# Optimization experiments

Hardware: AMD Instinct MI355X
Metric: run time of the kernel (lower is better)

The kernel has to match this reference:

```python
import jax, jax.numpy as jnp
import numpy as np

NUM_CLASSES = 21
THRESHOLD = 0.5
VAR0, VAR1 = 0.1, 0.2
NEGPOS_RATIO = 3


def setup_inputs() -> dict:
    key = jax.random.key(0)
    k1, k2, k3, k4, k5, k6, k7 = jax.random.split(key, 7)
    B, P, C, O = 64, 8732, 21, 8
    loc_data = jax.random.normal(k1, (B, P, 4), dtype=jnp.float32) * 0.1
    conf_data = jax.random.normal(k2, (B, P, C), dtype=jnp.float32)
    # priors: center form (cx, cy, w, h), valid in [0,1]
    cxy = jax.random.uniform(k3, (P, 2), minval=0.05, maxval=0.95)
    pwh = jax.random.uniform(k4, (P, 2), minval=0.05, maxval=0.3)
    priors = jnp.concatenate([cxy, pwh], axis=-1).astype(jnp.float32)
    # targets: corner-form boxes + class label (float), (B, O, 5)
    tc = jax.random.uniform(k5, (B, O, 2), minval=0.2, maxval=0.8)
    twh = jax.random.uniform(k6, (B, O, 2), minval=0.1, maxval=0.4)
    tmin = jnp.clip(tc - twh / 2, 0.0, 1.0)
    tmax = jnp.clip(tc + twh / 2, 0.0, 1.0)
    labels = jax.random.randint(k7, (B, O, 1), 0, C - 1).astype(jnp.float32)
    targets = jnp.concatenate([tmin, tmax, labels], axis=-1)
    return {"loc_data": loc_data, "conf_data": conf_data, "priors": priors, "targets": targets}


def _point_form(p):
    # (cx,cy,w,h) -> (xmin,ymin,xmax,ymax)
    return jnp.concatenate([p[:, :2] - p[:, 2:] / 2, p[:, :2] + p[:, 2:] / 2], axis=-1)


def _jaccard(a, b):
    # a: (O,4) corners, b: (P,4) corners -> (O,P)
    lt = jnp.maximum(a[:, None, :2], b[None, :, :2])
    rb = jnp.minimum(a[:, None, 2:], b[None, :, 2:])
    wh = jnp.clip(rb - lt, 0.0, None)
    inter = wh[..., 0] * wh[..., 1]
    area_a = ((a[:, 2] - a[:, 0]) * (a[:, 3] - a[:, 1]))[:, None]
    area_b = ((b[:, 2] - b[:, 0]) * (b[:, 3] - b[:, 1]))[None, :]
    return inter / (area_a + area_b - inter)


def _match_one(truths, labels, priors_pt, priors):
    # truths: (O,4) corners, labels: (O,), priors: (P,4) center-form
    ov = _jaccard(truths, priors_pt)                      # (O,P)
    best_prior_idx = jnp.argmax(ov, axis=1)               # (O,)
    best_truth_overlap = jnp.max(ov, axis=0)              # (P,)
    best_truth_idx = jnp.argmax(ov, axis=0)               # (P,)
    # ensure every gt box matches its best prior
    best_truth_overlap = best_truth_overlap.at[best_prior_idx].set(2.0)
    best_truth_idx = best_truth_idx.at[best_prior_idx].set(jnp.arange(truths.shape[0]))
    matched = truths[best_truth_idx]                      # (P,4)
    conf = labels[best_truth_idx].astype(jnp.int32) + 1
    conf = jnp.where(best_truth_overlap < THRESHOLD, 0, conf)
    # encode offsets
    g_cxcy = ((matched[:, :2] + matched[:, 2:]) / 2 - priors[:, :2]) / (VAR0 * priors[:, 2:])
    g_wh = jnp.log(jnp.clip((matched[:, 2:] - matched[:, :2]) / priors[:, 2:], 1e-8, None)) / VAR1
    return jnp.concatenate([g_cxcy, g_wh], axis=-1), conf


def _forward(loc_data, conf_data, priors, targets):
    B, P, C = conf_data.shape
    priors_sg = jax.lax.stop_gradient(priors)             # torch uses .data
    targets_sg = jax.lax.stop_gradient(targets)
    priors_pt = _point_form(priors_sg)
    loc_t, conf_t = jax.vmap(_match_one, in_axes=(0, 0, None, None))(
        targets_sg[:, :, :4], targets_sg[:, :, 4], priors_pt, priors_sg)
    pos = conf_t > 0                                      # (B,P)

    # localization: smooth L1 summed over positive priors
    diff = loc_data - loc_t
    ad = jnp.abs(diff)
    sl1 = jnp.where(ad < 1.0, 0.5 * diff * diff, ad - 0.5)
    loss_l = jnp.sum(sl1 * pos[..., None].astype(sl1.dtype))

    # per-prior conf loss for hard negative mining
    lse = jax.nn.logsumexp(conf_data, axis=-1)            # (B,P)
    gathered = jnp.take_along_axis(conf_data, conf_t[..., None], axis=-1)[..., 0]
    loss_c_all = lse - gathered                           # (B,P)
    mined = jnp.where(pos, 0.0, loss_c_all)
    loss_idx = jnp.argsort(-mined, axis=1)                # descending
    idx_rank = jnp.argsort(loss_idx, axis=1)
    num_pos = jnp.sum(pos.astype(jnp.int32), axis=1, keepdims=True)  # (B,1)
    num_neg = jnp.minimum(NEGPOS_RATIO * num_pos, P - num_pos)
    neg = idx_rank < num_neg                              # (B,P)

    sel = (pos | neg).astype(loss_c_all.dtype)
    loss_c = jnp.sum(loss_c_all * sel)

    N = jnp.sum(num_pos).astype(loss_l.dtype)
    return loss_l / N, loss_c / N


def reference(loc_data, conf_data, priors, targets):
    return _forward(loc_data, conf_data, priors, targets)
```

## Files before the change

kernel.cpp:

```cpp
#include <hip/hip_runtime.h>
#include <math.h>

#define TPB 256
#define CHP 512
#define TPBS 1024
#define RCAP 12

typedef unsigned long long ull;
typedef float pf4 __attribute__((ext_vector_type(4), aligned(4)));

__device__ __forceinline__ float jac(float tx0, float ty0, float tx1, float ty1, float ta,
                                     float px0, float py0, float px1, float py1, float pa) {
    float ltx = fmaxf(tx0, px0), lty = fmaxf(ty0, py0);
    float rbx = fminf(tx1, px1), rby = fminf(ty1, py1);
    float w = fmaxf(rbx - ltx, 0.0f), h = fmaxf(rby - lty, 0.0f);
    float inter = w * h;
    return inter / (ta + pa - inter);
}

template <int ON>
__global__ __launch_bounds__(TPB) void match1_kernel(
    const float* __restrict__ priors, const float* __restrict__ targets,
    int P, int O_rt, int S1, ull* __restrict__ pkeys) {
    constexpr int OMAX = (ON > 0) ? ON : 64;
    const int O = (ON > 0) ? ON : O_rt;
    const int b = blockIdx.x / S1;
    const int chunk = blockIdx.x % S1;
    const int p0 = chunk * CHP;
    const int p1 = min(p0 + CHP, P);
    const int tid = threadIdx.x;
    const int lane = tid & 63, wv = tid >> 6;

    __shared__ float s_tx0[OMAX], s_ty0[OMAX], s_tx1[OMAX], s_ty1[OMAX], s_area[OMAX];
    __shared__ ull s_wk[TPB / 64][OMAX];
    for (int o = tid; o < O; o += TPB) {
        const float* t = targets + ((size_t)b * O + o) * 5;
        float x0 = t[0], y0 = t[1], x1 = t[2], y1 = t[3];
        s_tx0[o] = x0; s_ty0[o] = y0; s_tx1[o] = x1; s_ty1[o] = y1;
        s_area[o] = (x1 - x0) * (y1 - y0);
    }
    __syncthreads();

    ull k[OMAX];
    for (int o = 0; o < O; ++o) k[o] = 0ull;
    for (int p = p0 + tid; p < p1; p += TPB) {
        float4 pr = ((const float4*)priors)[p];
        float px0 = pr.x - pr.z * 0.5f, py0 = pr.y - pr.w * 0.5f;
        float px1 = pr.x + pr.z * 0.5f, py1 = pr.y + pr.w * 0.5f;
        float pa = (px1 - px0) * (py1 - py0);
        for (int o = 0; o < O; ++o) {
            float ov = jac(s_tx0[o], s_ty0[o], s_tx1[o], s_ty1[o], s_area[o],
                           px0, py0, px1, py1, pa);
            ull kk = ((ull)__float_as_uint(ov) << 32) |
                     (ull)(0xFFFFFFFFu - (unsigned)p);
            if (kk > k[o]) k[o] = kk;
        }
    }
    for (int o = 0; o < O; ++o) {
        ull kk = k[o];
        for (int off = 32; off > 0; off >>= 1) {
            ull other = __shfl_down(kk, off, 64);
            if (other > kk) kk = other;
        }
        if (lane == 0) s_wk[wv][o] = kk;
    }
    __syncthreads();
    if (tid < O) {
        ull kk = s_wk[0][tid];
        for (int w = 1; w < TPB / 64; ++w)
            if (s_wk[w][tid] > kk) kk = s_wk[w][tid];
        pkeys[((size_t)b * O + tid) * S1 + chunk] = kk;
    }
}

template <int ON, int CN>
__global__ __launch_bounds__(TPB) void m2c_kernel(
    const float* __restrict__ loc, const float* __restrict__ priors,
    const float* __restrict__ targets, const float* __restrict__ conf,
    const ull* __restrict__ pkeys,
    int P, int O_rt, int C_rt, int S1, int CB2,
    float* __restrict__ mined, float* __restrict__ part_ll,
    float* __restrict__ part_pc, int* __restrict__ part_np) {
    constexpr int OMAX = (ON > 0) ? ON : 64;
    constexpr int CC = (CN > 0) ? CN : 32;
    const int O = (ON > 0) ? ON : O_rt;
    const int C = (CN > 0) ? CN : C_rt;
    const int b = blockIdx.x / CB2;
    const int chunk = blockIdx.x % CB2;
    const int tid = threadIdx.x;
    const int p = chunk * TPB + tid;
    const bool pv = (p < P);

    __shared__ float s_tx0[OMAX], s_ty0[OMAX], s_tx1[OMAX], s_ty1[OMAX];
    __shared__ float s_lab[OMAX], s_area[OMAX];
    __shared__ ull s_keys[OMAX];
    __shared__ int s_bp[OMAX];
    __shared__ float s_wll[TPB / 64], s_wpc[TPB / 64];
    __shared__ int s_wnp[TPB / 64];

    float rv[CC];
    float4 pr4 = make_float4(0.f, 0.f, 1.f, 1.f);
    if (pv) {
        const float* row = conf + ((size_t)b * P + p) * C;
        if (CN > 0) {
#pragma unroll
            for (int q = 0; q < CN / 4; ++q) {
                pf4 v = *(const pf4*)(row + 4 * q);
#pragma unroll
                for (int e = 0; e < 4; ++e) rv[4 * q + e] = v[e];
            }
#pragma unroll
            for (int j = (CN / 4) * 4; j < CN; ++j) rv[j] = row[j];
        } else {
            for (int j = 0; j < C; ++j) rv[j] = row[j];
        }
        pr4 = ((const float4*)priors)[p];
    }

    for (int o = tid; o < O; o += TPB) {
        const float* t = targets + ((size_t)b * O + o) * 5;
        float x0 = t[0], y0 = t[1], x1 = t[2], y1 = t[3];
        s_tx0[o] = x0; s_ty0[o] = y0; s_tx1[o] = x1; s_ty1[o] = y1;
        s_lab[o] = t[4];
        s_area[o] = (x1 - x0) * (y1 - y0);
        s_keys[o] = 0ull;
    }
    __syncthreads();
    if (tid < O * S1) {
        int o = tid / S1, s = tid % S1;
        atomicMax(&s_keys[o], pkeys[((size_t)b * O + o) * S1 + s]);
    }
    __syncthreads();
    if (tid < O)
        s_bp[tid] = (int)(0xFFFFFFFFu - (unsigned)(s_keys[tid] & 0xFFFFFFFFull));
    __syncthreads();

    float ll = 0.0f, pc = 0.0f;
    int np = 0;

    if (pv) {
        float m = rv[0];
#pragma unroll
        for (int j = 1; j < CC; ++j) { if (CN > 0 || j < C) m = fmaxf(m, rv[j]); }
        float s = 0.0f;
#pragma unroll
        for (int j = 0; j < CC; ++j) { if (CN > 0 || j < C) s += expf(rv[j] - m); }
        float lse = m + logf(s);

        float cx = pr4.x, cy = pr4.y, pw = pr4.z, ph = pr4.w;
        float px0 = cx - pw * 0.5f, py0 = cy - ph * 0.5f;
        float px1 = cx + pw * 0.5f, py1 = cy + ph * 0.5f;
        float pa = (px1 - px0) * (py1 - py0);
        float bto = -1.0f;
        int bti = 0;
        for (int o = 0; o < O; ++o) {
            float ov = jac(s_tx0[o], s_ty0[o], s_tx1[o], s_ty1[o], s_area[o],
                           px0, py0, px1, py1, pa);
            if (ov > bto) { bto = ov; bti = o; }
        }
        for (int o = 0; o < O; ++o) {
            if (s_bp[o] == p) { bto = 2.0f; bti = o; }
        }
        int c = (bto < 0.5f) ? 0 : ((int)s_lab[bti] + 1);

        float rowc = rv[0];
#pragma unroll
        for (int j = 1; j < CC; ++j) { if (CN > 0 || j < C) { if (c == j) rowc = rv[j]; } }
        float lc = lse - rowc;

        bool pos = c > 0;
        mined[(size_t)b * P + p] = pos ? 0.0f : lc;
        if (pos) {
            pc = lc;
            np = 1;
            float mx0 = s_tx0[bti], my0 = s_ty0[bti];
            float mx1 = s_tx1[bti], my1 = s_ty1[bti];
            float g0 = ((mx0 + mx1) * 0.5f - cx) / (0.1f * pw);
            float g1 = ((my0 + my1) * 0.5f - cy) / (0.1f * ph);
            float g2 = logf(fmaxf((mx1 - mx0) / pw, 1e-8f)) / 0.2f;
            float g3 = logf(fmaxf((my1 - my0) / ph, 1e-8f)) / 0.2f;
            float4 ld = ((const float4*)loc)[(size_t)b * P + p];
            float gt4[4] = {g0, g1, g2, g3};
            float lv[4] = {ld.x, ld.y, ld.z, ld.w};
#pragma unroll
            for (int q = 0; q < 4; ++q) {
                float d = lv[q] - gt4[q];
                float ad = fabsf(d);
                ll += (ad < 1.0f) ? 0.5f * d * d : (ad - 0.5f);
            }
        }
    }

#pragma unroll
    for (int d = 1; d < 64; d <<= 1) {
        ll += __shfl_xor(ll, d, 64);
        pc += __shfl_xor(pc, d, 64);
        np += __shfl_xor(np, d, 64);
    }
    const int wv = tid >> 6, lane = tid & 63;
    if (lane == 0) { s_wll[wv] = ll; s_wpc[wv] = pc; s_wnp[wv] = np; }
    __syncthreads();
    if (tid == 0) {
        float L = 0.f, Pc = 0.f;
        int N = 0;
        for (int w = 0; w < TPB / 64; ++w) { L += s_wll[w]; Pc += s_wpc[w]; N += s_wnp[w]; }
        part_ll[blockIdx.x] = L;
        part_pc[blockIdx.x] = Pc;
        part_np[blockIdx.x] = N;
    }
}

__global__ __launch_bounds__(TPBS) void select_kernel(
    const float* __restrict__ mined, const float* __restrict__ part_ll,
    const float* __restrict__ part_pc, const int* __restrict__ part_np,
    float* __restrict__ ll_batch, float* __restrict__ lc_batch,
    int* __restrict__ np_batch, int P, int CB, int ratio) {
    const int b = blockIdx.x, tid = threadIdx.x;
    const int lane = tid & 63, wv = tid >> 6;
    constexpr int W = TPBS / 64;
    const float* v = mined + (size_t)b * P;
    const int NIT = (P + TPBS - 1) / TPBS;
    const bool cached = (NIT <= RCAP);

    __shared__ float s_wf[W], s_wg[W];
    __shared__ int s_wi[W];
    __shared__ int s_hist[W * 256];
    __shared__ int s_wt[4];
    __shared__ unsigned s_bsel;
    __shared__ int s_krn;
    __shared__ float s_bc[2];
    __shared__ int s_bn;

    float rv[RCAP];
    if (cached) {
        for (int it = 0; it < NIT; ++it) {
            int p = tid + it * TPBS;
            rv[it] = (p < P) ? v[p] : 0.0f;
        }
    }

    float pll = 0.0f, ppc = 0.0f;
    int pnp = 0;
    for (int i = tid; i < CB; i += TPBS) {
        pll += part_ll[b * CB + i];
        ppc += part_pc[b * CB + i];
        pnp += part_np[b * CB + i];
    }
#pragma unroll
    for (int d = 1; d < 64; d <<= 1) {
        pll += __shfl_xor(pll, d, 64);
        ppc += __shfl_xor(ppc, d, 64);
        pnp += __shfl_xor(pnp, d, 64);
    }
    if (lane == 0) { s_wf[wv] = pll; s_wg[wv] = ppc; s_wi[wv] = pnp; }
    __syncthreads();
    if (tid == 0) {
        float L = 0.f, Pc = 0.f;
        int N = 0;
        for (int w = 0; w < W; ++w) { L += s_wf[w]; Pc += s_wg[w]; N += s_wi[w]; }
        s_bc[0] = L; s_bc[1] = Pc; s_bn = N;
    }
    __syncthreads();
    const float ll_sum = s_bc[0];
    const float sum_pos = s_bc[1];
    const int npos = s_bn;

    const int k = min(ratio * npos, P - npos);
    if (tid == 0) {
        ll_batch[b] = ll_sum;
        np_batch[b] = npos;
    }
    if (k <= 0) {
        if (tid == 0) lc_batch[b] = sum_pos;
        return;
    }

    unsigned prefix = 0u;
    int kr = k;
    for (int pass = 0; pass < 4; ++pass) {
        const int shift = 24 - 8 * pass;
        const unsigned mask = (pass == 0) ? 0u : (0xFFFFFFFFu << (32 - 8 * pass));
        for (int i = tid; i < W * 256; i += TPBS) s_hist[i] = 0;
        __syncthreads();
        for (int it = 0; it < NIT; ++it) {
            int p = tid + it * TPBS;
            if (p < P) {
                unsigned u = __float_as_uint(cached ? rv[it] : v[p]);
                if ((u & mask) == prefix)
                    atomicAdd(&s_hist[wv * 256 + ((u >> shift) & 0xFF)], 1);
            }
        }
        __syncthreads();
        int sge = 0, h = 0;
        if (tid < 256) {
            for (int w = 0; w < W; ++w) h += s_hist[w * 256 + tid];
            int val = h;
#pragma unroll
            for (int d = 1; d < 64; d <<= 1) {
                int t = __shfl_down(val, d, 64);
                if (lane + d < 64) val += t;
            }
            if (lane == 0) s_wt[tid >> 6] = val;
            sge = val;
        }
        __syncthreads();
        if (tid < 256) {
            for (int w = (tid >> 6) + 1; w < 4; ++w) sge += s_wt[w];
            int sgt = sge - h;
            if (sge >= kr && sgt < kr) {
                s_bsel = (unsigned)tid;
                s_krn = kr - sgt;
            }
        }
        __syncthreads();
        prefix |= s_bsel << shift;
        kr = s_krn;
    }
    const float T = __uint_as_float(prefix);
    float lsum = 0.0f;
    int lcnt = 0;
    for (int it = 0; it < NIT; ++it) {
        int p = tid + it * TPBS;
        if (p < P) {
            float x = cached ? rv[it] : v[p];
            if (x > T) { lsum += x; ++lcnt; }
        }
    }
#pragma unroll
    for (int d = 1; d < 64; d <<= 1) {
        lsum += __shfl_xor(lsum, d, 64);
        lcnt += __shfl_xor(lcnt, d, 64);
    }
    if (lane == 0) { s_wf[wv] = lsum; s_wi[wv] = lcnt; }
    __syncthreads();
    if (tid == 0) {
        float S = 0.f;
        int Cn = 0;
        for (int w = 0; w < W; ++w) { S += s_wf[w]; Cn += s_wi[w]; }
        lc_batch[b] = sum_pos + S + (float)(k - Cn) * T;
    }
}

__global__ __launch_bounds__(TPB) void finalize_kernel(
    const float* __restrict__ ll_batch, const int* __restrict__ np_batch,
    const float* __restrict__ lc_batch, int B, float* __restrict__ out) {
    const int tid = threadIdx.x;
    __shared__ float s_l[TPB], s_c[TPB];
    __shared__ int s_n[TPB];
    float l = 0.0f, c = 0.0f;
    int n = 0;
    for (int i = tid; i < B; i += TPB) {
        l += ll_batch[i];
        c += lc_batch[i];
        n += np_batch[i];
    }
    s_l[tid] = l; s_c[tid] = c; s_n[tid] = n;
    __syncthreads();
    for (int s = TPB / 2; s > 0; s >>= 1) {
        if (tid < s) {
            s_l[tid] += s_l[tid + s];
            s_c[tid] += s_c[tid + s];
            s_n[tid] += s_n[tid + s];
        }
        __syncthreads();
    }
    if (tid == 0) {
        float N = (float)s_n[0];
        out[0] = s_l[0] / N;
        out[1] = s_c[0] / N;
    }
}

extern "C" void kernel_launch(void* const* d_in, const int* in_sizes, int n_in,
                              void* d_out, int out_size, void* d_ws, size_t ws_size,
                              hipStream_t stream) {
    const float* loc = (const float*)d_in[0];
    const float* conf = (const float*)d_in[1];
    const float* priors = (const float*)d_in[2];
    const float* targets = (const float*)d_in[3];

    const int P = in_sizes[2] / 4;
    const int B = in_sizes[0] / (P * 4);
    const int C = in_sizes[1] / (in_sizes[0] / 4);
    const int O = in_sizes[3] / (B * 5);
    const size_t BP = (size_t)B * P;
    const int S1 = (P + CHP - 1) / CHP;
    const int CB2 = (P + TPB - 1) / TPB;

    ull* pkeys = (ull*)d_ws;
    float* mined = (float*)(pkeys + (size_t)B * O * S1);
    float* part_ll = mined + BP;
    float* part_pc = part_ll + (size_t)B * CB2;
    int* part_np = (int*)(part_pc + (size_t)B * CB2);
    float* ll_batch = (float*)(part_np + (size_t)B * CB2);
    float* lc_batch = ll_batch + B;
    int* np_batch = (int*)(lc_batch + B);

    if (O == 8) {
        match1_kernel<8><<<B * S1, TPB, 0, stream>>>(priors, targets, P, O, S1, pkeys);
        if (C == 21) {
            m2c_kernel<8, 21><<<B * CB2, TPB, 0, stream>>>(
                loc, priors, targets, conf, pkeys, P, O, C, S1, CB2,
                mined, part_ll, part_pc, part_np);
        } else {
            m2c_kernel<8, 0><<<B * CB2, TPB, 0, stream>>>(
                loc, priors, targets, conf, pkeys, P, O, C, S1, CB2,
                mined, part_ll, part_pc, part_np);
        }
    } else {
        match1_kernel<0><<<B * S1, TPB, 0, stream>>>(priors, targets, P, O, S1, pkeys);
        m2c_kernel<0, 0><<<B * CB2, TPB, 0, stream>>>(
            loc, priors, targets, conf, pkeys, P, O, C, S1, CB2,
            mined, part_ll, part_pc, part_np);
    }

    select_kernel<<<B, TPBS, 0, stream>>>(mined, part_ll, part_pc, part_np,
                                          ll_batch, lc_batch, np_batch, P, CB2, 3);

    finalize_kernel<<<1, TPB, 0, stream>>>(ll_batch, np_batch, lc_batch, B,
                                           (float*)d_out);
}
```

Baseline: 133.1 us.

## Fuse prior matching into conf kernel and patch forced matches in select

The separate match1 pass is removed. The conf/loss kernel now computes the per-truth best-prior keys itself and writes them out per block. The select kernel reduces those keys, applies the forced best-prior assignments as a delta correction to the loss sums, and zeroes those entries in the mined values. The finalize kernel is folded into select through a last-block atomic counter, so two launches and one pass over the priors are dropped. The cost is a more complex correction step: ownership dedup when several truths pick the same prior, an uncached path that rechecks forced priors, and a more intricate grid-wide completion protocol.

Result: slower. 162.1 us (+21.8%).

```diff
diff --git a/kernel.cpp b/kernel.cpp
--- a/kernel.cpp
+++ b/kernel.cpp
@@ -2,7 +2,6 @@
 #include <math.h>
 
 #define TPB 256
-#define CHP 512
 #define TPBS 1024
 #define RCAP 12
 
@@ -18,69 +17,14 @@
     return inter / (ta + pa - inter);
 }
 
-template <int ON>
-__global__ __launch_bounds__(TPB) void match1_kernel(
-    const float* __restrict__ priors, const float* __restrict__ targets,
-    int P, int O_rt, int S1, ull* __restrict__ pkeys) {
-    constexpr int OMAX = (ON > 0) ? ON : 64;
-    const int O = (ON > 0) ? ON : O_rt;
-    const int b = blockIdx.x / S1;
-    const int chunk = blockIdx.x % S1;
-    const int p0 = chunk * CHP;
-    const int p1 = min(p0 + CHP, P);
-    const int tid = threadIdx.x;
-    const int lane = tid & 63, wv = tid >> 6;
-
-    __shared__ float s_tx0[OMAX], s_ty0[OMAX], s_tx1[OMAX], s_ty1[OMAX], s_area[OMAX];
-    __shared__ ull s_wk[TPB / 64][OMAX];
-    for (int o = tid; o < O; o += TPB) {
-        const float* t = targets + ((size_t)b * O + o) * 5;
-        float x0 = t[0], y0 = t[1], x1 = t[2], y1 = t[3];
-        s_tx0[o] = x0; s_ty0[o] = y0; s_tx1[o] = x1; s_ty1[o] = y1;
-        s_area[o] = (x1 - x0) * (y1 - y0);
-    }
-    __syncthreads();
-
-    ull k[OMAX];
-    for (int o = 0; o < O; ++o) k[o] = 0ull;
-    for (int p = p0 + tid; p < p1; p += TPB) {
-        float4 pr = ((const float4*)priors)[p];
-        float px0 = pr.x - pr.z * 0.5f, py0 = pr.y - pr.w * 0.5f;
-        float px1 = pr.x + pr.z * 0.5f, py1 = pr.y + pr.w * 0.5f;
-        float pa = (px1 - px0) * (py1 - py0);
-        for (int o = 0; o < O; ++o) {
-            float ov = jac(s_tx0[o], s_ty0[o], s_tx1[o], s_ty1[o], s_area[o],
-                           px0, py0, px1, py1, pa);
-            ull kk = ((ull)__float_as_uint(ov) << 32) |
-                     (ull)(0xFFFFFFFFu - (unsigned)p);
-            if (kk > k[o]) k[o] = kk;
-        }
-    }
-    for (int o = 0; o < O; ++o) {
-        ull kk = k[o];
-        for (int off = 32; off > 0; off >>= 1) {
-            ull other = __shfl_down(kk, off, 64);
-            if (other > kk) kk = other;
-        }
-        if (lane == 0) s_wk[wv][o] = kk;
-    }
-    __syncthreads();
-    if (tid < O) {
-        ull kk = s_wk[0][tid];
-        for (int w = 1; w < TPB / 64; ++w)
-            if (s_wk[w][tid] > kk) kk = s_wk[w][tid];
-        pkeys[((size_t)b * O + tid) * S1 + chunk] = kk;
-    }
-}
-
 template <int ON, int CN>
-__global__ __launch_bounds__(TPB) void m2c_kernel(
+__global__ __launch_bounds__(TPB) void fused_kernel(
     const float* __restrict__ loc, const float* __restrict__ priors,
     const float* __restrict__ targets, const float* __restrict__ conf,
-    const ull* __restrict__ pkeys,
-    int P, int O_rt, int C_rt, int S1, int CB2,
-    float* __restrict__ mined, float* __restrict__ part_ll,
-    float* __restrict__ part_pc, int* __restrict__ part_np) {
+    int P, int O_rt, int C_rt, int CB2,
+    float* __restrict__ mined, ull* __restrict__ pkeys,
+    float* __restrict__ part_ll, float* __restrict__ part_pc,
+    int* __restrict__ part_np, int* __restrict__ counter) {
     constexpr int OMAX = (ON > 0) ? ON : 64;
     constexpr int CC = (CN > 0) ? CN : 32;
     const int O = (ON > 0) ? ON : O_rt;
@@ -90,11 +34,13 @@
     const int tid = threadIdx.x;
     const int p = chunk * TPB + tid;
     const bool pv = (p < P);
+    const int lane = tid & 63, wv = tid >> 6;
+
+    if (blockIdx.x == 0 && tid == 0) *counter = 0;
 
     __shared__ float s_tx0[OMAX], s_ty0[OMAX], s_tx1[OMAX], s_ty1[OMAX];
     __shared__ float s_lab[OMAX], s_area[OMAX];
-    __shared__ ull s_keys[OMAX];
-    __shared__ int s_bp[OMAX];
+    __shared__ ull s_wk[TPB / 64][OMAX];
     __shared__ float s_wll[TPB / 64], s_wpc[TPB / 64];
     __shared__ int s_wnp[TPB / 64];
 
@@ -123,21 +69,41 @@
         s_tx0[o] = x0; s_ty0[o] = y0; s_tx1[o] = x1; s_ty1[o] = y1;
         s_lab[o] = t[4];
         s_area[o] = (x1 - x0) * (y1 - y0);
-        s_keys[o] = 0ull;
-    }
-    __syncthreads();
-    if (tid < O * S1) {
-        int o = tid / S1, s = tid % S1;
-        atomicMax(&s_keys[o], pkeys[((size_t)b * O + o) * S1 + s]);
-    }
-    __syncthreads();
-    if (tid < O)
-        s_bp[tid] = (int)(0xFFFFFFFFu - (unsigned)(s_keys[tid] & 0xFFFFFFFFull));
-    __syncthreads();
+    }
+    __syncthreads();
+
+    float cx = pr4.x, cy = pr4.y, pw = pr4.z, ph = pr4.w;
+    float px0 = cx - pw * 0.5f, py0 = cy - ph * 0.5f;
+    float px1 = cx + pw * 0.5f, py1 = cy + ph * 0.5f;
+    float pa = (px1 - px0) * (py1 - py0);
+    float bto = -1.0f;
+    int bti = 0;
+    for (int o = 0; o < O; ++o) {
+        ull kk = 0ull;
+        if (pv) {
+            float ov = jac(s_tx0[o], s_ty0[o], s_tx1[o], s_ty1[o], s_area[o],
+                           px0, py0, px1, py1, pa);
+            kk = ((ull)__float_as_uint(ov) << 32) |
+                 (ull)(0xFFFFFFFFu - (unsigned)p);
+            if (ov > bto) { bto = ov; bti = o; }
+        }
+#pragma unroll
+        for (int d = 1; d < 64; d <<= 1) {
+            ull other = __shfl_xor(kk, d, 64);
+            if (other > kk) kk = other;
+        }
+        if (lane == 0) s_wk[wv][o] = kk;
+    }
+    __syncthreads();
+    if (tid < O) {
+        ull kk = s_wk[0][tid];
+        for (int w = 1; w < TPB / 64; ++w)
+            if (s_wk[w][tid] > kk) kk = s_wk[w][tid];
+        pkeys[((size_t)b * O + tid) * CB2 + chunk] = kk;
+    }
 
     float ll = 0.0f, pc = 0.0f;
     int np = 0;
-
     if (pv) {
         float m = rv[0];
 #pragma unroll
@@ -147,22 +113,7 @@
         for (int j = 0; j < CC; ++j) { if (CN > 0 || j < C) s += expf(rv[j] - m); }
         float lse = m + logf(s);
 
-        float cx = pr4.x, cy = pr4.y, pw = pr4.z, ph = pr4.w;
-        float px0 = cx - pw * 0.5f, py0 = cy - ph * 0.5f;
-        float px1 = cx + pw * 0.5f, py1 = cy + ph * 0.5f;
-        float pa = (px1 - px0) * (py1 - py0);
-        float bto = -1.0f;
-        int bti = 0;
-        for (int o = 0; o < O; ++o) {
-            float ov = jac(s_tx0[o], s_ty0[o], s_tx1[o], s_ty1[o], s_area[o],
-                           px0, py0, px1, py1, pa);
-            if (ov > bto) { bto = ov; bti = o; }
-        }
-        for (int o = 0; o < O; ++o) {
-            if (s_bp[o] == p) { bto = 2.0f; bti = o; }
-        }
         int c = (bto < 0.5f) ? 0 : ((int)s_lab[bti] + 1);
-
         float rowc = rv[0];
 #pragma unroll
         for (int j = 1; j < CC; ++j) { if (CN > 0 || j < C) { if (c == j) rowc = rv[j]; } }
@@ -197,7 +148,6 @@
         pc += __shfl_xor(pc, d, 64);
         np += __shfl_xor(np, d, 64);
     }
-    const int wv = tid >> 6, lane = tid & 63;
     if (lane == 0) { s_wll[wv] = ll; s_wpc[wv] = pc; s_wnp[wv] = np; }
     __syncthreads();
     if (tid == 0) {
@@ -210,11 +160,20 @@
     }
 }
 
+template <int ON, int CN>
 __global__ __launch_bounds__(TPBS) void select_kernel(
-    const float* __restrict__ mined, const float* __restrict__ part_ll,
-    const float* __restrict__ part_pc, const int* __restrict__ part_np,
+    const float* __restrict__ mined, const float* __restrict__ conf,
+    const float* __restrict__ loc, const float* __restrict__ priors,
+    const float* __restrict__ targets, const ull* __restrict__ pkeys,
+    const float* __restrict__ part_ll, const float* __restrict__ part_pc,
+    const int* __restrict__ part_np,
     float* __restrict__ ll_batch, float* __restrict__ lc_batch,
-    int* __restrict__ np_batch, int P, int CB, int ratio) {
+    int* __restrict__ np_batch,
+    int P, int O_rt, int C_rt, int CB2, int ratio, int B,
+    int* __restrict__ counter, float* __restrict__ out) {
+    constexpr int OMAX = (ON > 0) ? ON : 64;
+    const int O = (ON > 0) ? ON : O_rt;
+    const int C = (CN > 0) ? CN : C_rt;
     const int b = blockIdx.x, tid = threadIdx.x;
     const int lane = tid & 63, wv = tid >> 6;
     constexpr int W = TPBS / 64;
@@ -222,14 +181,18 @@
     const int NIT = (P + TPBS - 1) / TPBS;
     const bool cached = (NIT <= RCAP);
 
+    __shared__ float s_tx0[OMAX], s_ty0[OMAX], s_tx1[OMAX], s_ty1[OMAX];
+    __shared__ float s_lab[OMAX], s_area[OMAX];
+    __shared__ ull s_keys[OMAX];
+    __shared__ int s_bp[OMAX];
     __shared__ float s_wf[W], s_wg[W];
     __shared__ int s_wi[W];
     __shared__ int s_hist[W * 256];
     __shared__ int s_wt[4];
     __shared__ unsigned s_bsel;
     __shared__ int s_krn;
-    __shared__ float s_bc[2];
-    __shared__ int s_bn;
+    __shared__ float s_bc[2], s_fix[2];
+    __shared__ int s_bn, s_fixn, s_last;
 
     float rv[RCAP];
     if (cached) {
@@ -238,14 +201,42 @@
             rv[it] = (p < P) ? v[p] : 0.0f;
         }
     }
-
     float pll = 0.0f, ppc = 0.0f;
     int pnp = 0;
-    for (int i = tid; i < CB; i += TPBS) {
-        pll += part_ll[b * CB + i];
-        ppc += part_pc[b * CB + i];
-        pnp += part_np[b * CB + i];
-    }
+    for (int i = tid; i < CB2; i += TPBS) {
+        pll += part_ll[b * CB2 + i];
+        ppc += part_pc[b * CB2 + i];
+        pnp += part_np[b * CB2 + i];
+    }
+
+    if (tid < O) {
+        const float* t = targets + ((size_t)b * O + tid) * 5;
+        float x0 = t[0], y0 = t[1], x1 = t[2], y1 = t[3];
+        s_tx0[tid] = x0; s_ty0[tid] = y0; s_tx1[tid] = x1; s_ty1[tid] = y1;
+        s_lab[tid] = t[4];
+        s_area[tid] = (x1 - x0) * (y1 - y0);
+        s_keys[tid] = 0ull;
+    }
+    __syncthreads();
+    if (tid < O * CB2) {
+        int o = tid / CB2, s = tid % CB2;
+        atomicMax(&s_keys[o], pkeys[((size_t)b * O + o) * CB2 + s]);
+    }
+    __syncthreads();
+    if (tid < O)
+        s_bp[tid] = (int)(0xFFFFFFFFu - (unsigned)(s_keys[tid] & 0xFFFFFFFFull));
+    __syncthreads();
+
+    if (cached) {
+        for (int it = 0; it < NIT; ++it) {
+            int p = tid + it * TPBS;
+            if (p < P) {
+                for (int o = 0; o < O; ++o)
+                    if (p == s_bp[o]) rv[it] = 0.0f;
+            }
+        }
+    }
+
 #pragma unroll
     for (int d = 1; d < 64; d <<= 1) {
         pll += __shfl_xor(pll, d, 64);
@@ -253,12 +244,86 @@
         pnp += __shfl_xor(pnp, d, 64);
     }
     if (lane == 0) { s_wf[wv] = pll; s_wg[wv] = ppc; s_wi[wv] = pnp; }
+
+    float dll = 0.0f, dpc = 0.0f;
+    int dnp = 0;
+    if (tid < O) {
+        const int o = tid;
+        const int p = s_bp[o];
+        bool owner = true;
+        for (int o2 = o + 1; o2 < O; ++o2)
+            if (s_bp[o2] == p) owner = false;
+        if (owner) {
+            float4 pr = ((const float4*)priors)[p];
+            float cx = pr.x, cy = pr.y, pw = pr.z, ph = pr.w;
+            float px0 = cx - pw * 0.5f, py0 = cy - ph * 0.5f;
+            float px1 = cx + pw * 0.5f, py1 = cy + ph * 0.5f;
+            float pa = (px1 - px0) * (py1 - py0);
+            float bto = -1.0f;
+            int bti = 0;
+            for (int o2 = 0; o2 < O; ++o2) {
+                float ov = jac(s_tx0[o2], s_ty0[o2], s_tx1[o2], s_ty1[o2], s_area[o2],
+                               px0, py0, px1, py1, pa);
+                if (ov > bto) { bto = ov; bti = o2; }
+            }
+            int c_t = (bto < 0.5f) ? 0 : ((int)s_lab[bti] + 1);
+            const float* row = conf + ((size_t)b * P + p) * C;
+            float m = row[0];
+            for (int j = 1; j < C; ++j) m = fmaxf(m, row[j]);
+            float s = 0.0f;
+            for (int j = 0; j < C; ++j) s += expf(row[j] - m);
+            float lse = m + logf(s);
+            int c_n = (int)s_lab[o] + 1;
+            float lc_n = lse - row[c_n];
+            bool pos_t = c_t > 0;
+            float lc_t = lse - row[c_t];
+            dpc = lc_n - (pos_t ? lc_t : 0.0f);
+            dnp = 1 - (pos_t ? 1 : 0);
+            float4 ld = ((const float4*)loc)[(size_t)b * P + p];
+            float lv[4] = {ld.x, ld.y, ld.z, ld.w};
+            float sl_new = 0.0f, sl_old = 0.0f;
+            {
+                float mx0 = s_tx0[o], my0 = s_ty0[o], mx1 = s_tx1[o], my1 = s_ty1[o];
+                float g[4] = {((mx0 + mx1) * 0.5f - cx) / (0.1f * pw),
+                              ((my0 + my1) * 0.5f - cy) / (0.1f * ph),
+                              logf(fmaxf((mx1 - mx0) / pw, 1e-8f)) / 0.2f,
+                              logf(fmaxf((my1 - my0) / ph, 1e-8f)) / 0.2f};
+                for (int q = 0; q < 4; ++q) {
+                    float d = lv[q] - g[q];
+                    float ad = fabsf(d);
+                    sl_new += (ad < 1.0f) ? 0.5f * d * d : (ad - 0.5f);
+                }
+            }
+            if (pos_t) {
+                float mx0 = s_tx0[bti], my0 = s_ty0[bti], mx1 = s_tx1[bti], my1 = s_ty1[bti];
+                float g[4] = {((mx0 + mx1) * 0.5f - cx) / (0.1f * pw),
+                              ((my0 + my1) * 0.5f - cy) / (0.1f * ph),
+                              logf(fmaxf((mx1 - mx0) / pw, 1e-8f)) / 0.2f,
+                              logf(fmaxf((my1 - my0) / ph, 1e-8f)) / 0.2f};
+                for (int q = 0; q < 4; ++q) {
+                    float d = lv[q] - g[q];
+                    float ad = fabsf(d);
+                    sl_old += (ad < 1.0f) ? 0.5f * d * d : (ad - 0.5f);
+                }
+            }
+            dll = sl_new - sl_old;
+        }
+    }
+    if (wv == 0) {
+#pragma unroll
+        for (int d = 1; d < 64; d <<= 1) {
+            dll += __shfl_xor(dll, d, 64);
+            dpc += __shfl_xor(dpc, d, 64);
+            dnp += __shfl_xor(dnp, d, 64);
+        }
+        if (lane == 0) { s_fix[0] = dll; s_fix[1] = dpc; s_fixn = dnp; }
+    }
     __syncthreads();
     if (tid == 0) {
         float L = 0.f, Pc = 0.f;
         int N = 0;
         for (int w = 0; w < W; ++w) { L += s_wf[w]; Pc += s_wg[w]; N += s_wi[w]; }
-        s_bc[0] = L; s_bc[1] = Pc; s_bn = N;
+        s_bc[0] = L + s_fix[0]; s_bc[1] = Pc + s_fix[1]; s_bn = N + s_fixn;
     }
     __syncthreads();
     const float ll_sum = s_bc[0];
@@ -270,104 +335,120 @@
         ll_batch[b] = ll_sum;
         np_batch[b] = npos;
     }
+
     if (k <= 0) {
         if (tid == 0) lc_batch[b] = sum_pos;
-        return;
-    }
-
-    unsigned prefix = 0u;
-    int kr = k;
-    for (int pass = 0; pass < 4; ++pass) {
-        const int shift = 24 - 8 * pass;
-        const unsigned mask = (pass == 0) ? 0u : (0xFFFFFFFFu << (32 - 8 * pass));
-        for (int i = tid; i < W * 256; i += TPBS) s_hist[i] = 0;
-        __syncthreads();
+    } else {
+        unsigned prefix = 0u;
+        int kr = k;
+        for (int pass = 0; pass < 4; ++pass) {
+            const int shift = 24 - 8 * pass;
+            const unsigned mask = (pass == 0) ? 0u : (0xFFFFFFFFu << (32 - 8 * pass));
+            for (int i = tid; i < W * 256; i += TPBS) s_hist[i] = 0;
+            __syncthreads();
+            for (int it = 0; it < NIT; ++it) {
+                int p = tid + it * TPBS;
+                if (p < P) {
+                    float x;
+                    if (cached) x = rv[it];
+                    else {
+                        x = v[p];
+                        for (int o = 0; o < O; ++o)
+                            if (p == s_bp[o]) x = 0.0f;
+                    }
+                    unsigned u = __float_as_uint(x);
+                    if ((u & mask) == prefix)
+                        atomicAdd(&s_hist[wv * 256 + ((u >> shift) & 0xFF)], 1);
+                }
+            }
+            __syncthreads();
+            int sge = 0, h = 0;
+            if (tid < 256) {
+                for (int w = 0; w < W; ++w) h += s_hist[w * 256 + tid];
+                int val = h;
+#pragma unroll
+                for (int d = 1; d < 64; d <<= 1) {
+                    int t = __shfl_down(val, d, 64);
+                    if (lane + d < 64) val += t;
+                }
+                if (lane == 0) s_wt[tid >> 6] = val;
+                sge = val;
+            }
+            __syncthreads();
+            if (tid < 256) {
+                for (int w = (tid >> 6) + 1; w < 4; ++w) sge += s_wt[w];
+                int sgt = sge - h;
+                if (sge >= kr && sgt < kr) {
+                    s_bsel = (unsigned)tid;
+                    s_krn = kr - sgt;
+                }
+            }
+            __syncthreads();
+            prefix |= s_bsel << shift;
+            kr = s_krn;
+        }
+        const float T = __uint_as_float(prefix);
+        float lsum = 0.0f;
+        int lcnt = 0;
         for (int it = 0; it < NIT; ++it) {
             int p = tid + it * TPBS;
             if (p < P) {
-                unsigned u = __float_as_uint(cached ? rv[it] : v[p]);
-                if ((u & mask) == prefix)
-                    atomicAdd(&s_hist[wv * 256 + ((u >> shift) & 0xFF)], 1);
-            }
-        }
+                float x;
+                if (cached) x = rv[it];
+                else {
+                    x = v[p];
+                    for (int o = 0; o < O; ++o)
+                        if (p == s_bp[o]) x = 0.0f;
+                }
+                if (x > T) { lsum += x; ++lcnt; }
+            }
+        }
+#pragma unroll
+        for (int d = 1; d < 64; d <<= 1) {
+            lsum += __shfl_xor(lsum, d, 64);
+            lcnt += __shfl_xor(lcnt, d, 64);
+        }
+        if (lane == 0) { s_wf[wv] = lsum; s_wi[wv] = lcnt; }
         __syncthreads();
-        int sge = 0, h = 0;
-        if (tid < 256) {
-            for (int w = 0; w < W; ++w) h += s_hist[w * 256 + tid];
-            int val = h;
-#pragma unroll
-            for (int d = 1; d < 64; d <<= 1) {
-                int t = __shfl_down(val, d, 64);
-                if (lane + d < 64) val += t;
-            }
-            if (lane == 0) s_wt[tid >> 6] = val;
-            sge = val;
-        }
+        if (tid == 0) {
+            float S = 0.f;
+            int Cn = 0;
+            for (int w = 0; w < W; ++w) { S += s_wf[w]; Cn += s_wi[w]; }
+            lc_batch[b] = sum_pos + S + (float)(k - Cn) * T;
+        }
+    }
+
+    __threadfence();
+    if (tid == 0) {
+        int old = atomicAdd(counter, 1);
+        s_last = (old == B - 1) ? 1 : 0;
+    }
+    __syncthreads();
+    if (s_last) {
+        __threadfence();
+        float l = 0.0f, c = 0.0f;
+        int n = 0;
+        for (int i = tid; i < B; i += TPBS) {
+            l += ll_batch[i];
+            c += lc_batch[i];
+            n += np_batch[i];
+        }
+#pragma unroll
+        for (int d = 1; d < 64; d <<= 1) {
+            l += __shfl_xor(l, d, 64);
+            c += __shfl_xor(c, d, 64);
+            n += __shfl_xor(n, d, 64);
+        }
+        if (lane == 0) { s_wf[wv] = l; s_wg[wv] = c; s_wi[wv] = n; }
         __syncthreads();
-        if (tid < 256) {
-            for (int w = (tid >> 6) + 1; w < 4; ++w) sge += s_wt[w];
-            int sgt = sge - h;
-            if (sge >= kr && sgt < kr) {
-                s_bsel = (unsigned)tid;
-                s_krn = kr - sgt;
-            }
-        }
-        __syncthreads();
-        prefix |= s_bsel << shift;
-        kr = s_krn;
-    }
-    const float T = __uint_as_float(prefix);
-    float lsum = 0.0f;
-    int lcnt = 0;
-    for (int it = 0; it < NIT; ++it) {
-        int p = tid + it * TPBS;
-        if (p < P) {
-            float x = cached ? rv[it] : v[p];
-            if (x > T) { lsum += x; ++lcnt; }
-        }
-    }
-#pragma unroll
-    for (int d = 1; d < 64; d <<= 1) {
-        lsum += __shfl_xor(lsum, d, 64);
-        lcnt += __shfl_xor(lcnt, d, 64);
-    }
-    if (lane == 0) { s_wf[wv] = lsum; s_wi[wv] = lcnt; }
-    __syncthreads();
-    if (tid == 0) {
-        float S = 0.f;
-        int Cn = 0;
-        for (int w = 0; w < W; ++w) { S += s_wf[w]; Cn += s_wi[w]; }
-        lc_batch[b] = sum_pos + S + (float)(k - Cn) * T;
-    }
-}
-
-__global__ __launch_bounds__(TPB) void finalize_kernel(
-    const float* __restrict__ ll_batch, const int* __restrict__ np_batch,
-    const float* __restrict__ lc_batch, int B, float* __restrict__ out) {
-    const int tid = threadIdx.x;
-    __shared__ float s_l[TPB], s_c[TPB];
-    __shared__ int s_n[TPB];
-    float l = 0.0f, c = 0.0f;
-    int n = 0;
-    for (int i = tid; i < B; i += TPB) {
-        l += ll_batch[i];
-        c += lc_batch[i];
-        n += np_batch[i];
-    }
-    s_l[tid] = l; s_c[tid] = c; s_n[tid] = n;
-    __syncthreads();
-    for (int s = TPB / 2; s > 0; s >>= 1) {
-        if (tid < s) {
-            s_l[tid] += s_l[tid + s];
-            s_c[tid] += s_c[tid + s];
-            s_n[tid] += s_n[tid + s];
-        }
-        __syncthreads();
-    }
-    if (tid == 0) {
-        float N = (float)s_n[0];
-        out[0] = s_l[0] / N;
-        out[1] = s_c[0] / N;
+        if (tid == 0) {
+            float L = 0.f, Cc = 0.f;
+            int N = 0;
+            for (int w = 0; w < W; ++w) { L += s_wf[w]; Cc += s_wg[w]; N += s_wi[w]; }
+            float Nf = (float)N;
+            out[0] = L / Nf;
+            out[1] = Cc / Nf;
+        }
     }
 }
 
@@ -384,39 +465,31 @@
     const int C = in_sizes[1] / (in_sizes[0] / 4);
     const int O = in_sizes[3] / (B * 5);
     const size_t BP = (size_t)B * P;
-    const int S1 = (P + CHP - 1) / CHP;
     const int CB2 = (P + TPB - 1) / TPB;
 
     ull* pkeys = (ull*)d_ws;
-    float* mined = (float*)(pkeys + (size_t)B * O * S1);
+    float* mined = (float*)(pkeys + (size_t)B * O * CB2);
     float* part_ll = mined + BP;
     float* part_pc = part_ll + (size_t)B * CB2;
     int* part_np = (int*)(part_pc + (size_t)B * CB2);
     float* ll_batch = (float*)(part_np + (size_t)B * CB2);
     float* lc_batch = ll_batch + B;
     int* np_batch = (int*)(lc_batch + B);
-
-    if (O == 8) {
-        match1_kernel<8><<<B * S1, TPB, 0, stream>>>(priors, targets, P, O, S1, pkeys);
-        if (C == 21) {
-            m2c_kernel<8, 21><<<B * CB2, TPB, 0, stream>>>(
-                loc, priors, targets, conf, pkeys, P, O, C, S1, CB2,
-                mined, part_ll, part_pc, part_np);
-        } else {
-            m2c_kernel<8, 0><<<B * CB2, TPB, 0, stream>>>(
-                loc, priors, targets, conf, pkeys, P, O, C, S1, CB2,
-                mined, part_ll, part_pc, part_np);
-        }
+    int* counter = np_batch + B;
+
+    if (O == 8 && C == 21) {
+        fused_kernel<8, 21><<<B * CB2, TPB, 0, stream>>>(
+            loc, priors, targets, conf, P, O, C, CB2,
+            mined, pkeys, part_ll, part_pc, part_np, counter);
+        select_kernel<8, 21><<<B, TPBS, 0, stream>>>(
+            mined, conf, loc, priors, targets, pkeys, part_ll, part_pc, part_np,
+            ll_batch, lc_batch, np_batch, P, O, C, CB2, 3, B, counter, (float*)d_out);
     } else {
-        match1_kernel<0><<<B * S1, TPB, 0, stream>>>(priors, targets, P, O, S1, pkeys);
-        m2c_kernel<0, 0><<<B * CB2, TPB, 0, stream>>>(
-            loc, priors, targets, conf, pkeys, P, O, C, S1, CB2,
-            mined, part_ll, part_pc, part_np);
-    }
-
-    select_kernel<<<B, TPBS, 0, stream>>>(mined, part_ll, part_pc, part_np,
-                                          ll_batch, lc_batch, np_batch, P, CB2, 3);
-
-    finalize_kernel<<<1, TPB, 0, stream>>>(ll_batch, np_batch, lc_batch, B,
-                                           (float*)d_out);
+        fused_kernel<0, 0><<<B * CB2, TPB, 0, stream>>>(
+            loc, priors, targets, conf, P, O, C, CB2,
+            mined, pkeys, part_ll, part_pc, part_np, counter);
+        select_kernel<0, 0><<<B, TPBS, 0, stream>>>(
+            mined, conf, loc, priors, targets, pkeys, part_ll, part_pc, part_np,
+            ll_batch, lc_batch, np_batch, P, O, C, CB2, 3, B, counter, (float*)d_out);
+    }
 }
```
